# Kernel optimization log

Measured on AMD Instinct MI355X. Metric: run time of the kernel, lower is better.

Reference implementation:

```python
import jax, jax.numpy as jnp
import numpy as np

BITS = 4
GROUP = 128
M, K, N = 16, 4096, 11008


def setup_inputs() -> dict:
    key = jax.random.key(0)
    k1, k2, k3 = jax.random.split(key, 3)
    A = jax.random.normal(k1, (M, K), dtype=jnp.float16)
    # packed 4-bit weights: 2 nibbles per byte, stored as int32 holding 0..255
    qweight = jax.random.randint(k2, (N, K * BITS // 8), 0, 256, dtype=jnp.int32)
    # small positive-ish scales like real GPTQ checkpoints
    scales = (jax.random.normal(k3, (N, K // GROUP)) * 0.01 + 0.02).astype(jnp.float16)
    zeros = jnp.zeros((N, K // GROUP), dtype=jnp.float16)
    bias = jnp.zeros((N,), dtype=jnp.float16)
    return {"A": A, "qweight": qweight, "scales": scales, "zeros": zeros, "bias": bias}


def _dequant(qweight, scales, zeros):
    # qweight: (N, K//2) packed; element idx -> byte idx//2, low nibble if idx even
    low = qweight & 0xF
    high = (qweight >> 4) & 0xF
    w_int = jnp.stack([low, high], axis=-1).reshape(qweight.shape[0], -1)  # (N, K)
    # per-group dequant with 'original' zeros: W = (q - z) * s
    s = jnp.repeat(scales, GROUP, axis=1)  # (N, K)
    z = jnp.repeat(zeros, GROUP, axis=1)   # (N, K)
    return (w_int.astype(jnp.float16) - z) * s


def reference(A, qweight, scales, zeros, bias):
    W = _dequant(qweight, scales, zeros)           # (N, K) fp16
    return jnp.matmul(A, W.T) + bias               # (M, N) fp16
```

## Files before the change

### kernel.cpp

```cpp
#include <hip/hip_runtime.h>

#define KK 4096
#define NN 11008
#define NGRP 32
#define KW (KK / 2)
#define ROWB 8192
#define LROW 528
#define TILEB (16 * LROW)
#define WS_RS_OFF 131072

using short8  = __attribute__((ext_vector_type(8))) short;
using float4v = __attribute__((ext_vector_type(4))) float;

static __device__ __forceinline__ unsigned int pack_bf16(float lo, float hi) {
    unsigned int ul = __builtin_bit_cast(unsigned int, lo);
    unsigned int uh = __builtin_bit_cast(unsigned int, hi);
    ul = (ul + 0x7FFFu + ((ul >> 16) & 1u)) >> 16;
    uh = (uh + 0x7FFFu + ((uh >> 16) & 1u)) & 0xFFFF0000u;
    return ul | uh;
}
static __device__ __forceinline__ float bf16val(float f) {
    unsigned int u = __builtin_bit_cast(unsigned int, f);
    u = (u + 0x7FFFu + ((u >> 16) & 1u)) & 0xFFFF0000u;
    return __builtin_bit_cast(float, u);
}

__global__ __launch_bounds__(256) void prep_kernel(
    const float* __restrict__ A, unsigned short* __restrict__ wsA,
    float* __restrict__ rowsum)
{
    const int b = blockIdx.x;
    if (b < 32) {
        const int idx = (b * 256 + threadIdx.x) * 8;
        float4v x0 = *(const float4v*)(A + idx);
        float4v x1 = *(const float4v*)(A + idx + 4);
        union { short8 s8; unsigned int u[4]; } p;
        p.u[0] = pack_bf16(x0[0], x0[1]);
        p.u[1] = pack_bf16(x0[2], x0[3]);
        p.u[2] = pack_bf16(x1[0], x1[1]);
        p.u[3] = pack_bf16(x1[2], x1[3]);
        *(short8*)(wsA + idx) = p.s8;
    } else {
        const int sid = (b - 32) * 16 + (threadIdx.x >> 4);
        const int m = sid >> 5, g = sid & 31;
        const int j = threadIdx.x & 15;
        const float* p = A + (size_t)m * KK + g * 128 + j * 8;
        float4v x0 = *(const float4v*)p;
        float4v x1 = *(const float4v*)(p + 4);
        float sum = bf16val(x0[0]) + bf16val(x0[1]) + bf16val(x0[2]) + bf16val(x0[3])
                  + bf16val(x1[0]) + bf16val(x1[1]) + bf16val(x1[2]) + bf16val(x1[3]);
        sum += __shfl_xor(sum, 1, 16);
        sum += __shfl_xor(sum, 2, 16);
        sum += __shfl_xor(sum, 4, 16);
        sum += __shfl_xor(sum, 8, 16);
        if (j == 0) rowsum[sid] = sum;
    }
}

__global__ __launch_bounds__(256) void qgemm_kernel(
    const int*   __restrict__ qweight,
    const float* __restrict__ scales,
    const float* __restrict__ zeros,
    const float* __restrict__ bias,
    const unsigned short* __restrict__ wsA,
    const float* __restrict__ rowsum,
    float*       __restrict__ out)
{
    const int nt = blockIdx.x >> 1;
    const int kh = blockIdx.x & 1;
    const int n0 = nt * 16;
    const int wid  = threadIdx.x >> 6;
    const int lane = threadIdx.x & 63;
    const int nl   = lane & 15;
    const int quad = lane >> 4;

    __shared__ __align__(16) char lds[2 * TILEB];

    const char* qbase = (const char*)qweight + (size_t)n0 * ROWB + kh * 4096;
    const int   r0    = wid * 4 + (lane >> 5);
    const int   sbyte = (lane & 31) * 16;
    const char* gp0 = qbase + (size_t)r0 * ROWB + sbyte;
    const char* gp1 = qbase + (size_t)(r0 + 2) * ROWB + sbyte;
    char* lw0 = lds + r0 * LROW + sbyte;
    char* lw1 = lds + (r0 + 2) * LROW + sbyte;

    const unsigned short* arow = wsA + (size_t)nl * KK;
    const float*          srow = scales + (size_t)(n0 + nl) * NGRP + kh * 16;
    const char*           fr   = lds + nl * LROW + wid * 64 + quad * 16;

    int4 ra = *(const int4*)(gp0);
    int4 rb = *(const int4*)(gp1);

    float4v acc = {0.f, 0.f, 0.f, 0.f};

    for (int s = 0; s < 8; ++s) {
        const int bo = (s & 1) * TILEB;
        *(int4*)(lw0 + bo) = ra;
        *(int4*)(lw1 + bo) = rb;
        if (s < 7) {
            ra = *(const int4*)(gp0 + (s + 1) * 512);
            rb = *(const int4*)(gp1 + (s + 1) * 512);
        }
        __syncthreads();

        #pragma unroll
        for (int gg = 0; gg < 2; ++gg) {
            const int k0 = kh * 2048 + (s * 2 + gg) * 128 + wid * 32 + quad * 8;
            short8 a = *(const short8*)(arow + k0);
            int4 wv = *(const int4*)(fr + bo + gg * 256);
            union { short8 s8; unsigned int u[4]; } bf;
            const unsigned int w0 = (unsigned int)wv.x, w1 = (unsigned int)wv.y;
            const unsigned int w2 = (unsigned int)wv.z, w3 = (unsigned int)wv.w;
            bf.u[0] = (w0 & 0xFu) | ((w0 << 12) & 0x000F0000u) | 0x43004300u;
            bf.u[1] = (w1 & 0xFu) | ((w1 << 12) & 0x000F0000u) | 0x43004300u;
            bf.u[2] = (w2 & 0xFu) | ((w2 << 12) & 0x000F0000u) | 0x43004300u;
            bf.u[3] = (w3 & 0xFu) | ((w3 << 12) & 0x000F0000u) | 0x43004300u;
            float4v z4 = {0.f, 0.f, 0.f, 0.f};
            float4v accg = __builtin_amdgcn_mfma_f32_16x16x32_bf16(a, bf.s8, z4, 0, 0, 0);
            const float sg = srow[s * 2 + gg];
            #pragma unroll
            for (int r = 0; r < 4; ++r)
                acc[r] = __builtin_fmaf(sg, accg[r], acc[r]);
        }
    }

    __shared__ float red[4][16][16];
    #pragma unroll
    for (int r = 0; r < 4; ++r)
        red[wid][quad * 4 + r][nl] = acc[r];
    __syncthreads();

    const int t  = threadIdx.x;
    const int m  = t >> 4;
    const int nn = t & 15;
    const int ng = n0 + nn;
    float val = red[0][m][nn] + red[1][m][nn] + red[2][m][nn] + red[3][m][nn];

    const int gh0 = kh * 16;
    const float* sr  = scales + (size_t)ng * NGRP + gh0;
    const float* zr  = zeros  + (size_t)ng * NGRP + gh0;
    const float* rsm = rowsum + m * NGRP + gh0;
    float corr = 0.f;
    #pragma unroll
    for (int gg = 0; gg < 16; ++gg)
        corr = __builtin_fmaf(sr[gg] * (128.0f + zr[gg]), rsm[gg], corr);
    val -= corr;
    if (kh == 0) val += bias[ng];
    atomicAdd(&out[(size_t)m * NN + ng], val);
}

extern "C" void kernel_launch(void* const* d_in, const int* in_sizes, int n_in,
                              void* d_out, int out_size, void* d_ws, size_t ws_size,
                              hipStream_t stream) {
    const float* A       = (const float*)d_in[0];
    const int*   qweight = (const int*)d_in[1];
    const float* scales  = (const float*)d_in[2];
    const float* zeros   = (const float*)d_in[3];
    const float* bias    = (const float*)d_in[4];
    float*       out     = (float*)d_out;

    unsigned short* wsA = (unsigned short*)d_ws;
    float* rowsum       = (float*)((char*)d_ws + WS_RS_OFF);

    prep_kernel<<<dim3(64), dim3(256), 0, stream>>>(A, wsA, rowsum);
    qgemm_kernel<<<dim3(2 * NN / 16), dim3(256), 0, stream>>>(
        qweight, scales, zeros, bias, wsA, rowsum, out);
}
```

Measured before the change: 151.0 us.

## Split K into 8 slices, drop LDS staging, precompute zero-point correction

The GEMM now gives each block 8 K-slices of 16 output columns instead of 2, with one group per wave. Each wave reads its weights straight from global memory into registers, so the LDS double buffer and its barriers go away. A is pre-permuted into MFMA fragment order, and scale*(128+zero) is precomputed. A new init kernel writes bias minus the zero-point correction to the output before the atomic accumulation. This raises parallelism and removes per-block correction work, but costs an extra launch and four times more atomics.

```diff
diff --git a/kernel.cpp b/kernel.cpp
--- a/kernel.cpp
+++ b/kernel.cpp
@@ -3,11 +3,9 @@
 #define KK 4096
 #define NN 11008
 #define NGRP 32
-#define KW (KK / 2)
-#define ROWB 8192
-#define LROW 528
-#define TILEB (16 * LROW)
+#define KW 2048
 #define WS_RS_OFF 131072
+#define WS_SZ_OFF 139264
 
 using short8  = __attribute__((ext_vector_type(8))) short;
 using float4v = __attribute__((ext_vector_type(4))) float;
@@ -26,24 +24,26 @@
 }
 
 __global__ __launch_bounds__(256) void prep_kernel(
-    const float* __restrict__ A, unsigned short* __restrict__ wsA,
-    float* __restrict__ rowsum)
+    const float* __restrict__ A, const float* __restrict__ scales,
+    const float* __restrict__ zeros, unsigned short* __restrict__ wsA,
+    float* __restrict__ rowsum, float* __restrict__ SZ)
 {
-    const int b = blockIdx.x;
+    const int b = blockIdx.x, t = threadIdx.x;
     if (b < 32) {
-        const int idx = (b * 256 + threadIdx.x) * 8;
-        float4v x0 = *(const float4v*)(A + idx);
-        float4v x1 = *(const float4v*)(A + idx + 4);
+        const int tid = b * 256 + t;
+        const int c = tid >> 6, l = tid & 63;
+        const float* src = A + (size_t)(l & 15) * KK + c * 32 + (l >> 4) * 8;
+        float4v x0 = *(const float4v*)src;
+        float4v x1 = *(const float4v*)(src + 4);
         union { short8 s8; unsigned int u[4]; } p;
         p.u[0] = pack_bf16(x0[0], x0[1]);
         p.u[1] = pack_bf16(x0[2], x0[3]);
         p.u[2] = pack_bf16(x1[0], x1[1]);
         p.u[3] = pack_bf16(x1[2], x1[3]);
-        *(short8*)(wsA + idx) = p.s8;
-    } else {
-        const int sid = (b - 32) * 16 + (threadIdx.x >> 4);
-        const int m = sid >> 5, g = sid & 31;
-        const int j = threadIdx.x & 15;
+        *(short8*)(wsA + (size_t)tid * 8) = p.s8;
+    } else if (b < 64) {
+        const int sid = (b - 32) * 16 + (t >> 4);
+        const int m = sid >> 5, g = sid & 31, j = t & 15;
         const float* p = A + (size_t)m * KK + g * 128 + j * 8;
         float4v x0 = *(const float4v*)p;
         float4v x1 = *(const float4v*)(p + 4);
@@ -54,99 +54,87 @@
         sum += __shfl_xor(sum, 4, 16);
         sum += __shfl_xor(sum, 8, 16);
         if (j == 0) rowsum[sid] = sum;
+    } else {
+        const int e0 = (b - 64) * 1024 + t * 4;
+        float4v s4 = *(const float4v*)(scales + e0);
+        float4v z4 = *(const float4v*)(zeros + e0);
+        float4v r;
+        #pragma unroll
+        for (int j = 0; j < 4; ++j) r[j] = s4[j] * (128.0f + z4[j]);
+        *(float4v*)(SZ + e0) = r;
     }
 }
 
+__global__ __launch_bounds__(256) void init_out_kernel(
+    const float* __restrict__ bias, const float* __restrict__ SZ,
+    const float* __restrict__ rowsum, float* __restrict__ out)
+{
+    __shared__ float rs[16][32];
+    const int t = threadIdx.x;
+    rs[t >> 5][t & 31]       = rowsum[t];
+    rs[(t >> 5) + 8][t & 31] = rowsum[t + 256];
+    __syncthreads();
+    const int n0 = blockIdx.x * 16;
+    const int m = t >> 4, nn = t & 15, ng = n0 + nn;
+    const float* szr = SZ + (size_t)ng * NGRP;
+    float corr = 0.f;
+    #pragma unroll
+    for (int g = 0; g < 32; ++g)
+        corr = __builtin_fmaf(szr[g], rs[m][g], corr);
+    out[(size_t)m * NN + ng] = bias[ng] - corr;
+}
+
 __global__ __launch_bounds__(256) void qgemm_kernel(
-    const int*   __restrict__ qweight,
-    const float* __restrict__ scales,
-    const float* __restrict__ zeros,
-    const float* __restrict__ bias,
-    const unsigned short* __restrict__ wsA,
-    const float* __restrict__ rowsum,
-    float*       __restrict__ out)
+    const int*            __restrict__ qweight,
+    const float*          __restrict__ scales,
+    const unsigned short* __restrict__ aperm,
+    float*                __restrict__ out)
 {
-    const int nt = blockIdx.x >> 1;
-    const int kh = blockIdx.x & 1;
+    const int nt = blockIdx.x >> 3, slice = blockIdx.x & 7;
     const int n0 = nt * 16;
-    const int wid  = threadIdx.x >> 6;
-    const int lane = threadIdx.x & 63;
-    const int nl   = lane & 15;
-    const int quad = lane >> 4;
+    const int wid = threadIdx.x >> 6, lane = threadIdx.x & 63;
+    const int nl = lane & 15, quad = lane >> 4;
+    const int n = n0 + nl;
+    const int g = slice * 4 + wid;
 
-    __shared__ __align__(16) char lds[2 * TILEB];
+    const int* qrow = qweight + (size_t)n * KW + g * 64 + quad * 4;
+    const unsigned short* ap = aperm + (size_t)g * 2048 + lane * 8;
 
-    const char* qbase = (const char*)qweight + (size_t)n0 * ROWB + kh * 4096;
-    const int   r0    = wid * 4 + (lane >> 5);
-    const int   sbyte = (lane & 31) * 16;
-    const char* gp0 = qbase + (size_t)r0 * ROWB + sbyte;
-    const char* gp1 = qbase + (size_t)(r0 + 2) * ROWB + sbyte;
-    char* lw0 = lds + r0 * LROW + sbyte;
-    char* lw1 = lds + (r0 + 2) * LROW + sbyte;
-
-    const unsigned short* arow = wsA + (size_t)nl * KK;
-    const float*          srow = scales + (size_t)(n0 + nl) * NGRP + kh * 16;
-    const char*           fr   = lds + nl * LROW + wid * 64 + quad * 16;
-
-    int4 ra = *(const int4*)(gp0);
-    int4 rb = *(const int4*)(gp1);
+    int4   w0 = *(const int4*)(qrow);
+    int4   w1 = *(const int4*)(qrow + 16);
+    int4   w2 = *(const int4*)(qrow + 32);
+    int4   w3 = *(const int4*)(qrow + 48);
+    short8 a0 = *(const short8*)(ap);
+    short8 a1 = *(const short8*)(ap + 512);
+    short8 a2 = *(const short8*)(ap + 1024);
+    short8 a3 = *(const short8*)(ap + 1536);
+    const float s = scales[n * NGRP + g];
 
     float4v acc = {0.f, 0.f, 0.f, 0.f};
-
-    for (int s = 0; s < 8; ++s) {
-        const int bo = (s & 1) * TILEB;
-        *(int4*)(lw0 + bo) = ra;
-        *(int4*)(lw1 + bo) = rb;
-        if (s < 7) {
-            ra = *(const int4*)(gp0 + (s + 1) * 512);
-            rb = *(const int4*)(gp1 + (s + 1) * 512);
-        }
-        __syncthreads();
-
-        #pragma unroll
-        for (int gg = 0; gg < 2; ++gg) {
-            const int k0 = kh * 2048 + (s * 2 + gg) * 128 + wid * 32 + quad * 8;
-            short8 a = *(const short8*)(arow + k0);
-            int4 wv = *(const int4*)(fr + bo + gg * 256);
-            union { short8 s8; unsigned int u[4]; } bf;
-            const unsigned int w0 = (unsigned int)wv.x, w1 = (unsigned int)wv.y;
-            const unsigned int w2 = (unsigned int)wv.z, w3 = (unsigned int)wv.w;
-            bf.u[0] = (w0 & 0xFu) | ((w0 << 12) & 0x000F0000u) | 0x43004300u;
-            bf.u[1] = (w1 & 0xFu) | ((w1 << 12) & 0x000F0000u) | 0x43004300u;
-            bf.u[2] = (w2 & 0xFu) | ((w2 << 12) & 0x000F0000u) | 0x43004300u;
-            bf.u[3] = (w3 & 0xFu) | ((w3 << 12) & 0x000F0000u) | 0x43004300u;
-            float4v z4 = {0.f, 0.f, 0.f, 0.f};
-            float4v accg = __builtin_amdgcn_mfma_f32_16x16x32_bf16(a, bf.s8, z4, 0, 0, 0);
-            const float sg = srow[s * 2 + gg];
-            #pragma unroll
-            for (int r = 0; r < 4; ++r)
-                acc[r] = __builtin_fmaf(sg, accg[r], acc[r]);
-        }
+    int4 wv[4] = {w0, w1, w2, w3};
+    short8 av[4] = {a0, a1, a2, a3};
+    #pragma unroll
+    for (int t = 0; t < 4; ++t) {
+        const unsigned int x0 = (unsigned int)wv[t].x, x1 = (unsigned int)wv[t].y;
+        const unsigned int x2 = (unsigned int)wv[t].z, x3 = (unsigned int)wv[t].w;
+        union { short8 s8; unsigned int u[4]; } bf;
+        bf.u[0] = (x0 & 0xFu) | ((x0 << 12) & 0x000F0000u) | 0x43004300u;
+        bf.u[1] = (x1 & 0xFu) | ((x1 << 12) & 0x000F0000u) | 0x43004300u;
+        bf.u[2] = (x2 & 0xFu) | ((x2 << 12) & 0x000F0000u) | 0x43004300u;
+        bf.u[3] = (x3 & 0xFu) | ((x3 << 12) & 0x000F0000u) | 0x43004300u;
+        acc = __builtin_amdgcn_mfma_f32_16x16x32_bf16(av[t], bf.s8, acc, 0, 0, 0);
     }
 
     __shared__ float red[4][16][16];
     #pragma unroll
     for (int r = 0; r < 4; ++r)
-        red[wid][quad * 4 + r][nl] = acc[r];
+        red[wid][quad * 4 + r][nl] = s * acc[r];
     __syncthreads();
 
-    const int t  = threadIdx.x;
-    const int m  = t >> 4;
-    const int nn = t & 15;
-    const int ng = n0 + nn;
+    const int t = threadIdx.x;
+    const int m = t >> 4, nn = t & 15;
     float val = red[0][m][nn] + red[1][m][nn] + red[2][m][nn] + red[3][m][nn];
-
-    const int gh0 = kh * 16;
-    const float* sr  = scales + (size_t)ng * NGRP + gh0;
-    const float* zr  = zeros  + (size_t)ng * NGRP + gh0;
-    const float* rsm = rowsum + m * NGRP + gh0;
-    float corr = 0.f;
-    #pragma unroll
-    for (int gg = 0; gg < 16; ++gg)
-        corr = __builtin_fmaf(sr[gg] * (128.0f + zr[gg]), rsm[gg], corr);
-    val -= corr;
-    if (kh == 0) val += bias[ng];
-    atomicAdd(&out[(size_t)m * NN + ng], val);
+    atomicAdd(&out[(size_t)m * NN + n0 + nn], val);
 }
 
 extern "C" void kernel_launch(void* const* d_in, const int* in_sizes, int n_in,
@@ -161,8 +149,9 @@
 
     unsigned short* wsA = (unsigned short*)d_ws;
     float* rowsum       = (float*)((char*)d_ws + WS_RS_OFF);
+    float* SZ           = (float*)((char*)d_ws + WS_SZ_OFF);
 
-    prep_kernel<<<dim3(64), dim3(256), 0, stream>>>(A, wsA, rowsum);
-    qgemm_kernel<<<dim3(2 * NN / 16), dim3(256), 0, stream>>>(
-        qweight, scales, zeros, bias, wsA, rowsum, out);
+    prep_kernel<<<dim3(408), dim3(256), 0, stream>>>(A, scales, zeros, wsA, rowsum, SZ);
+    init_out_kernel<<<dim3(688), dim3(256), 0, stream>>>(bias, SZ, rowsum, out);
+    qgemm_kernel<<<dim3(5504), dim3(256), 0, stream>>>(qweight, scales, wsA, out);
 }
```

Result: faster. 144.3 us (-4.4%).
